# Performance work log

Measured on AMD Instinct MI355X. Metric: run time of the kernel, lower is better.

## Reference

```python
import jax, jax.numpy as jnp
import numpy as np

B, N, D = 1, 65536, 1024
H = 512
R = 16  # num_regions
C = 2   # num_classes

def _gelu(x):
    return jax.nn.gelu(x, approximate=False)  # torch nn.GELU default is exact erf

def setup_inputs() -> dict:
    key = jax.random.key(0)
    ks = jax.random.split(key, 16)
    s = 0.02
    return {
        "embeddings": jax.random.normal(ks[0], (B, N, D), dtype=jnp.float32),
        # region_encoder: Linear(D,H) + GELU (dropout=0 in eval)
        "W1": jax.random.normal(ks[1], (D, H), dtype=jnp.float32) * s,
        "b1": jnp.zeros((H,), dtype=jnp.float32),
        # region_attention: Linear(H,H//2) -> tanh -> Linear(H//2,1)
        "Wa1": jax.random.normal(ks[2], (H, H // 2), dtype=jnp.float32) * s,
        "ba1": jnp.zeros((H // 2,), dtype=jnp.float32),
        "Wa2": jax.random.normal(ks[3], (H // 2, 1), dtype=jnp.float32) * s,
        "ba2": jnp.zeros((1,), dtype=jnp.float32),
        # slide_encoder: Linear(H,H) + GELU
        "Ws": jax.random.normal(ks[4], (H, H), dtype=jnp.float32) * s,
        "bs": jnp.zeros((H,), dtype=jnp.float32),
        # slide_attention
        "Wsa1": jax.random.normal(ks[5], (H, H // 2), dtype=jnp.float32) * s,
        "bsa1": jnp.zeros((H // 2,), dtype=jnp.float32),
        "Wsa2": jax.random.normal(ks[6], (H // 2, 1), dtype=jnp.float32) * s,
        "bsa2": jnp.zeros((1,), dtype=jnp.float32),
        # classifier: Linear(H,H//2) -> GELU -> Linear(H//2,C)
        "Wc1": jax.random.normal(ks[7], (H, H // 2), dtype=jnp.float32) * s,
        "bc1": jnp.zeros((H // 2,), dtype=jnp.float32),
        "Wc2": jax.random.normal(ks[8], (H // 2, C), dtype=jnp.float32) * s,
        "bc2": jnp.zeros((C,), dtype=jnp.float32),
    }

def reference(embeddings, W1, b1, Wa1, ba1, Wa2, ba2, Ws, bs, Wsa1, bsa1, Wsa2, bsa2, Wc1, bc1, Wc2, bc2):
    b, n, d = embeddings.shape
    m = n // R  # patches per region
    # coords=None path: region_ids[i] = i % R, so region r holds indices r, r+R, ...
    # Equivalent regrouping via reshape+transpose: (B, M, R, D) -> (B, R, M, D)
    x = embeddings.reshape(b, m, R, d).transpose(0, 2, 1, 3)
    # region encoder
    region_emb = _gelu(jnp.einsum('brmd,dh->brmh', x, W1) + b1)  # (B,R,M,H)
    # region attention pooling
    scores = jnp.einsum('brmk,ko->brmo', jnp.tanh(jnp.einsum('brmh,hk->brmk', region_emb, Wa1) + ba1), Wa2) + ba2  # (B,R,M,1)
    attn = jax.nn.softmax(scores, axis=2)
    region_features = jnp.sum(region_emb * attn, axis=2)  # (B,R,H)
    # slide encoder + attention pooling over regions
    slide_emb = _gelu(jnp.einsum('brh,hg->brg', region_features, Ws) + bs)  # (B,R,H)
    sattn = jnp.einsum('brk,ko->bro', jnp.tanh(jnp.einsum('brh,hk->brk', slide_emb, Wsa1) + bsa1), Wsa2) + bsa2  # (B,R,1)
    sweights = jax.nn.softmax(sattn, axis=1)
    slide_rep = jnp.sum(slide_emb * sweights, axis=1)  # (B,H)
    # classifier
    logits = _gelu(slide_rep @ Wc1 + bc1) @ Wc2 + bc2  # (B,C)
    return logits
```

## Files before the change

kernel.cpp:

```cpp
#include <hip/hip_runtime.h>

#define NTOK 65536
#define DIN  1024
#define H    512
#define HH   256
#define NREG 16
#define MPR  4096

__device__ __forceinline__ unsigned short f2bf(float f) {
  unsigned u = __float_as_uint(f);
  u += 0x7fffu + ((u >> 16) & 1u);
  return (unsigned short)(u >> 16);
}
__device__ __forceinline__ float bf2f(unsigned short s) {
  return __uint_as_float(((unsigned)s) << 16);
}
__device__ __forceinline__ float gelu_exact(float x) {
  return 0.5f * x * (1.0f + erff(x * 0.70710678118654752440f));
}

typedef __attribute__((ext_vector_type(8))) short shortx8;
typedef __attribute__((ext_vector_type(4))) float floatx4;

__device__ __forceinline__ void gl_lds16(const void* g, void* l) {
  __builtin_amdgcn_global_load_lds(
      (const __attribute__((address_space(1))) void*)g,
      (__attribute__((address_space(3))) void*)l, 16, 0, 0);
}

__global__ __launch_bounds__(256) void k0_prep(const float* __restrict__ W1,
                                               const float* __restrict__ Wa1,
                                               unsigned short* __restrict__ W1t,
                                               unsigned short* __restrict__ Wa1t) {
  int idx = blockIdx.x * 256 + threadIdx.x;
  if (idx < DIN * H) {
    int n = idx >> 10, k = idx & 1023;
    W1t[idx] = f2bf(W1[k * H + n]);
  } else {
    int i2 = idx - DIN * H;
    int n = i2 >> 9, k = i2 & 511;
    Wa1t[i2] = f2bf(Wa1[k * HH + n]);
  }
}

__global__ __launch_bounds__(256) void k1_gemm1(const float* __restrict__ X,
                                                const unsigned short* __restrict__ W1t,
                                                const float* __restrict__ b1,
                                                unsigned short* __restrict__ Eb) {
  __shared__ __align__(16) short lA[128 * 32];
  __shared__ __align__(16) short lB[128 * 32];
  const int tid = threadIdx.x;
  const int colBase = blockIdx.x * 128;
  const int rowBase = blockIdx.y * 128;
  const int lane = tid & 63;
  const int wave = tid >> 6;
  const int wr = wave >> 1, wc = wave & 1;
  const int l15 = lane & 15, quad = lane >> 4;

  floatx4 acc[4][4] = {};

  for (int kb = 0; kb < DIN; kb += 32) {
    __syncthreads();
#pragma unroll
    for (int s = 0; s < 2; s++) {
      int c = tid + s * 256;
      gl_lds16(W1t + (size_t)(colBase + (c >> 2)) * DIN + kb + (c & 3) * 8, &lB[c * 8]);
    }
#pragma unroll
    for (int s = 0; s < 2; s++) {
      int c = tid + s * 256;
      const floatx4* src =
          (const floatx4*)(X + (size_t)(rowBase + (c >> 2)) * DIN + kb + (c & 3) * 8);
      floatx4 f0 = src[0], f1 = src[1];
      shortx8 h;
      h[0] = (short)f2bf(f0[0]); h[1] = (short)f2bf(f0[1]);
      h[2] = (short)f2bf(f0[2]); h[3] = (short)f2bf(f0[3]);
      h[4] = (short)f2bf(f1[0]); h[5] = (short)f2bf(f1[1]);
      h[6] = (short)f2bf(f1[2]); h[7] = (short)f2bf(f1[3]);
      *(shortx8*)(&lA[c * 8]) = h;
    }
    __syncthreads();
    shortx8 aF[4], bF[4];
#pragma unroll
    for (int i = 0; i < 4; i++)
      aF[i] = *(const shortx8*)(&lA[(wr * 64 + i * 16 + l15) * 32 + quad * 8]);
#pragma unroll
    for (int j = 0; j < 4; j++)
      bF[j] = *(const shortx8*)(&lB[(wc * 64 + j * 16 + l15) * 32 + quad * 8]);
#pragma unroll
    for (int i = 0; i < 4; i++)
#pragma unroll
      for (int j = 0; j < 4; j++)
        acc[i][j] = __builtin_amdgcn_mfma_f32_16x16x32_bf16(aF[i], bF[j], acc[i][j], 0, 0, 0);
  }

  const int row0 = rowBase + wr * 64;
  const int col0 = colBase + wc * 64;
#pragma unroll
  for (int j = 0; j < 4; j++) {
    int col = col0 + j * 16 + l15;
    float bias = b1[col];
#pragma unroll
    for (int i = 0; i < 4; i++) {
      int rb = row0 + i * 16 + quad * 4;
#pragma unroll
      for (int v = 0; v < 4; v++) {
        float x = acc[i][j][v] + bias;
        Eb[(size_t)(rb + v) * H + col] = f2bf(gelu_exact(x));
      }
    }
  }
}

__global__ __launch_bounds__(256) void k2_gemm2(const unsigned short* __restrict__ Eb,
                                                const unsigned short* __restrict__ Wa1t,
                                                const float* __restrict__ ba1,
                                                const float* __restrict__ Wa2,
                                                float* __restrict__ scores) {
  __shared__ __align__(16) short lA[128 * 32];
  __shared__ __align__(16) short lB[128 * 32];
  const int tid = threadIdx.x;
  const int colBase = blockIdx.x * 128;
  const int rowBase = blockIdx.y * 128;
  const int lane = tid & 63;
  const int wave = tid >> 6;
  const int wr = wave >> 1, wc = wave & 1;
  const int l15 = lane & 15, quad = lane >> 4;

  floatx4 acc[4][4] = {};

  for (int kb = 0; kb < H; kb += 32) {
    __syncthreads();
#pragma unroll
    for (int s = 0; s < 2; s++) {
      int c = tid + s * 256;
      gl_lds16(Eb + (size_t)(rowBase + (c >> 2)) * H + kb + (c & 3) * 8, &lA[c * 8]);
      gl_lds16(Wa1t + (size_t)(colBase + (c >> 2)) * H + kb + (c & 3) * 8, &lB[c * 8]);
    }
    __syncthreads();
    shortx8 aF[4], bF[4];
#pragma unroll
    for (int i = 0; i < 4; i++)
      aF[i] = *(const shortx8*)(&lA[(wr * 64 + i * 16 + l15) * 32 + quad * 8]);
#pragma unroll
    for (int j = 0; j < 4; j++)
      bF[j] = *(const shortx8*)(&lB[(wc * 64 + j * 16 + l15) * 32 + quad * 8]);
#pragma unroll
    for (int i = 0; i < 4; i++)
#pragma unroll
      for (int j = 0; j < 4; j++)
        acc[i][j] = __builtin_amdgcn_mfma_f32_16x16x32_bf16(aF[i], bF[j], acc[i][j], 0, 0, 0);
  }

  float p[4][4];
#pragma unroll
  for (int i = 0; i < 4; i++)
#pragma unroll
    for (int v = 0; v < 4; v++) p[i][v] = 0.0f;
#pragma unroll
  for (int j = 0; j < 4; j++) {
    int col = colBase + wc * 64 + j * 16 + l15;
    float bias = ba1[col];
    float wa2 = Wa2[col];
#pragma unroll
    for (int i = 0; i < 4; i++)
#pragma unroll
      for (int v = 0; v < 4; v++)
        p[i][v] += tanhf(acc[i][j][v] + bias) * wa2;
  }
#pragma unroll
  for (int i = 0; i < 4; i++)
#pragma unroll
    for (int v = 0; v < 4; v++) {
      float t = p[i][v];
      t += __shfl_xor(t, 1, 16);
      t += __shfl_xor(t, 2, 16);
      t += __shfl_xor(t, 4, 16);
      t += __shfl_xor(t, 8, 16);
      p[i][v] = t;
    }
  if (l15 == 0) {
    int row0 = rowBase + wr * 64 + quad * 4;
#pragma unroll
    for (int i = 0; i < 4; i++)
#pragma unroll
      for (int v = 0; v < 4; v++)
        atomicAdd(&scores[row0 + i * 16 + v], p[i][v]);
  }
}

__global__ __launch_bounds__(256) void k3a_softmax(const float* __restrict__ scores,
                                                   float* __restrict__ wts) {
  const int r = blockIdx.x, tid = threadIdx.x;
  __shared__ float red[256];
  float m = -1e30f;
  for (int j = tid; j < MPR; j += 256) m = fmaxf(m, scores[r + NREG * j]);
  red[tid] = m;
  __syncthreads();
  for (int s = 128; s > 0; s >>= 1) {
    if (tid < s) red[tid] = fmaxf(red[tid], red[tid + s]);
    __syncthreads();
  }
  float mx = red[0];
  __syncthreads();
  float sum = 0.0f;
  for (int j = tid; j < MPR; j += 256) sum += expf(scores[r + NREG * j] - mx);
  red[tid] = sum;
  __syncthreads();
  for (int s = 128; s > 0; s >>= 1) {
    if (tid < s) red[tid] += red[tid + s];
    __syncthreads();
  }
  float inv = 1.0f / red[0];
  for (int j = tid; j < MPR; j += 256)
    wts[r + NREG * j] = expf(scores[r + NREG * j] - mx) * inv;
}

__global__ __launch_bounds__(256) void k3b_wsum(const unsigned short* __restrict__ Eb,
                                                const float* __restrict__ wts,
                                                float* __restrict__ rf) {
  const int r = blockIdx.y;
  const int mc = blockIdx.x;
  const int tid = threadIdx.x;
  float a0 = 0.0f, a1 = 0.0f;
  for (int j = mc * 128; j < mc * 128 + 128; j++) {
    int n = r + NREG * j;
    float w = wts[n];
    unsigned v = *(const unsigned*)(Eb + (size_t)n * H + tid * 2);
    a0 += w * bf2f((unsigned short)(v & 0xffffu));
    a1 += w * bf2f((unsigned short)(v >> 16));
  }
  atomicAdd(&rf[r * H + tid * 2], a0);
  atomicAdd(&rf[r * H + tid * 2 + 1], a1);
}

__global__ __launch_bounds__(256) void k4a_slide(const float* __restrict__ rf,
                                                 const float* __restrict__ Ws,
                                                 const float* __restrict__ bs,
                                                 float* __restrict__ se) {
  const int r = blockIdx.x, tid = threadIdx.x;
  __shared__ float lrf[H];
  lrf[tid] = rf[r * H + tid];
  lrf[tid + 256] = rf[r * H + tid + 256];
  __syncthreads();
  float a0 = 0.0f, a1 = 0.0f;
  for (int k = 0; k < H; k++) {
    float x = lrf[k];
    a0 += x * Ws[k * H + tid];
    a1 += x * Ws[k * H + tid + 256];
  }
  se[r * H + tid] = gelu_exact(a0 + bs[tid]);
  se[r * H + tid + 256] = gelu_exact(a1 + bs[tid + 256]);
}

__global__ __launch_bounds__(256) void k4b_sscore(const float* __restrict__ se,
                                                  const float* __restrict__ Wsa1,
                                                  const float* __restrict__ bsa1,
                                                  const float* __restrict__ Wsa2,
                                                  const float* __restrict__ bsa2,
                                                  float* __restrict__ ss) {
  const int r = blockIdx.x, tid = threadIdx.x;
  __shared__ float lse[H];
  __shared__ float red[256];
  lse[tid] = se[r * H + tid];
  lse[tid + 256] = se[r * H + tid + 256];
  __syncthreads();
  float a = 0.0f;
  for (int k = 0; k < H; k++) a += lse[k] * Wsa1[k * HH + tid];
  red[tid] = tanhf(a + bsa1[tid]) * Wsa2[tid];
  __syncthreads();
  for (int s = 128; s > 0; s >>= 1) {
    if (tid < s) red[tid] += red[tid + s];
    __syncthreads();
  }
  if (tid == 0) ss[r] = red[0] + bsa2[0];
}

__global__ __launch_bounds__(256) void k4c_final(const float* __restrict__ se,
                                                 const float* __restrict__ ss,
                                                 const float* __restrict__ Wc1,
                                                 const float* __restrict__ bc1,
                                                 const float* __restrict__ Wc2,
                                                 const float* __restrict__ bc2,
                                                 float* __restrict__ out) {
  const int tid = threadIdx.x;
  __shared__ float srep[H];
  __shared__ float r0[256], r1[256];
  float mx = -1e30f;
  for (int i = 0; i < NREG; i++) mx = fmaxf(mx, ss[i]);
  float wv[NREG];
  float den = 0.0f;
  for (int i = 0; i < NREG; i++) { wv[i] = expf(ss[i] - mx); den += wv[i]; }
  float inv = 1.0f / den;
  float s0 = 0.0f, s1 = 0.0f;
  for (int i = 0; i < NREG; i++) {
    float w = wv[i] * inv;
    s0 += w * se[i * H + tid];
    s1 += w * se[i * H + tid + 256];
  }
  srep[tid] = s0;
  srep[tid + 256] = s1;
  __syncthreads();
  float a = 0.0f;
  for (int k = 0; k < H; k++) a += srep[k] * Wc1[k * HH + tid];
  float g = gelu_exact(a + bc1[tid]);
  r0[tid] = g * Wc2[tid * 2];
  r1[tid] = g * Wc2[tid * 2 + 1];
  __syncthreads();
  for (int s = 128; s > 0; s >>= 1) {
    if (tid < s) { r0[tid] += r0[tid + s]; r1[tid] += r1[tid + s]; }
    __syncthreads();
  }
  if (tid == 0) {
    out[0] = r0[0] + bc2[0];
    out[1] = r1[0] + bc2[1];
  }
}

extern "C" void kernel_launch(void* const* d_in, const int* in_sizes, int n_in,
                              void* d_out, int out_size, void* d_ws, size_t ws_size,
                              hipStream_t stream) {
  const float* X    = (const float*)d_in[0];
  const float* W1   = (const float*)d_in[1];
  const float* b1   = (const float*)d_in[2];
  const float* Wa1  = (const float*)d_in[3];
  const float* ba1  = (const float*)d_in[4];
  const float* Wa2  = (const float*)d_in[5];
  const float* Ws   = (const float*)d_in[7];
  const float* bs   = (const float*)d_in[8];
  const float* Wsa1 = (const float*)d_in[9];
  const float* bsa1 = (const float*)d_in[10];
  const float* Wsa2 = (const float*)d_in[11];
  const float* bsa2 = (const float*)d_in[12];
  const float* Wc1  = (const float*)d_in[13];
  const float* bc1  = (const float*)d_in[14];
  const float* Wc2  = (const float*)d_in[15];
  const float* bc2  = (const float*)d_in[16];
  float* out = (float*)d_out;

  char* ws = (char*)d_ws;
  constexpr size_t OFF_W1T  = 0;
  constexpr size_t OFF_WA1T = OFF_W1T + (size_t)H * DIN * 2;
  constexpr size_t OFF_EB   = OFF_WA1T + (size_t)HH * H * 2;
  constexpr size_t OFF_SC   = OFF_EB + (size_t)NTOK * H * 2;
  constexpr size_t OFF_RF   = OFF_SC + (size_t)NTOK * 4;
  constexpr size_t OFF_WT   = OFF_RF + (size_t)NREG * H * 4;
  constexpr size_t OFF_SE   = OFF_WT + (size_t)NTOK * 4;
  constexpr size_t OFF_SS   = OFF_SE + (size_t)NREG * H * 4;

  unsigned short* W1t  = (unsigned short*)(ws + OFF_W1T);
  unsigned short* Wa1t = (unsigned short*)(ws + OFF_WA1T);
  unsigned short* Eb   = (unsigned short*)(ws + OFF_EB);
  float* scores = (float*)(ws + OFF_SC);
  float* rf     = (float*)(ws + OFF_RF);
  float* wts    = (float*)(ws + OFF_WT);
  float* se     = (float*)(ws + OFF_SE);
  float* ssb    = (float*)(ws + OFF_SS);

  hipMemsetAsync(scores, 0, (size_t)NTOK * 4 + (size_t)NREG * H * 4, stream);

  k0_prep<<<(DIN * H + HH * H) / 256, 256, 0, stream>>>(W1, Wa1, W1t, Wa1t);
  k1_gemm1<<<dim3(4, 512), 256, 0, stream>>>(X, W1t, b1, Eb);
  k2_gemm2<<<dim3(2, 512), 256, 0, stream>>>(Eb, Wa1t, ba1, Wa2, scores);
  k3a_softmax<<<NREG, 256, 0, stream>>>(scores, wts);
  k3b_wsum<<<dim3(32, NREG), 256, 0, stream>>>(Eb, wts, rf);
  k4a_slide<<<NREG, 256, 0, stream>>>(rf, Ws, bs, se);
  k4b_sscore<<<NREG, 256, 0, stream>>>(se, Wsa1, bsa1, Wsa2, bsa2, ssb);
  k4c_final<<<1, 256, 0, stream>>>(se, ssb, Wc1, bc1, Wc2, bc2, out);
}
```

Before: 652.6 us.

## Widen GEMM1 tile to full H, swizzle LDS, use hardware bf16 convert and fast tanh

GEMM1 now uses 512-thread blocks that each compute a 128x512 output tile, so every block covers all of H. Each fp32 X row is then read and converted once instead of four times. LDS layouts in both GEMMs get an XOR swizzle to reduce bank conflicts on fragment reads. Hardware v_cvt_pk_bf16_f32 replaces the software rounding, and an exp/rcp tanh replaces tanhf in the score epilogue. The costs are much higher register pressure from 32 accumulators per wave, a larger LDS footprint, and a slightly less accurate tanh.

```diff
diff --git a/kernel.cpp b/kernel.cpp
--- a/kernel.cpp
+++ b/kernel.cpp
@@ -18,14 +18,33 @@
 __device__ __forceinline__ float gelu_exact(float x) {
   return 0.5f * x * (1.0f + erff(x * 0.70710678118654752440f));
 }
+__device__ __forceinline__ unsigned cvt_pk_bf16(float lo, float hi) {
+  unsigned r;
+  asm("v_cvt_pk_bf16_f32 %0, %1, %2" : "=v"(r) : "v"(lo), "v"(hi));
+  return r;
+}
+__device__ __forceinline__ unsigned short f2bf_hw(float f) {
+  unsigned r;
+  asm("v_cvt_pk_bf16_f32 %0, %1, %2" : "=v"(r) : "v"(f), "v"(f));
+  return (unsigned short)r;
+}
+__device__ __forceinline__ float fast_tanh(float x) {
+  float e = __expf(2.0f * x);
+  return 1.0f - 2.0f * __builtin_amdgcn_rcpf(e + 1.0f);
+}
 
 typedef __attribute__((ext_vector_type(8))) short shortx8;
 typedef __attribute__((ext_vector_type(4))) float floatx4;
+typedef __attribute__((ext_vector_type(4))) unsigned int uintx4;
 
 __device__ __forceinline__ void gl_lds16(const void* g, void* l) {
   __builtin_amdgcn_global_load_lds(
       (const __attribute__((address_space(1))) void*)g,
       (__attribute__((address_space(3))) void*)l, 16, 0, 0);
+}
+
+__device__ __forceinline__ int swz8(int row, int seg) {
+  return (row * 4 + (seg ^ ((row >> 1) & 3))) * 8;
 }
 
 __global__ __launch_bounds__(256) void k0_prep(const float* __restrict__ W1,
@@ -43,62 +62,67 @@
   }
 }
 
-__global__ __launch_bounds__(256) void k1_gemm1(const float* __restrict__ X,
+__global__ __launch_bounds__(512) void k1_gemm1(const float* __restrict__ X,
                                                 const unsigned short* __restrict__ W1t,
                                                 const float* __restrict__ b1,
                                                 unsigned short* __restrict__ Eb) {
   __shared__ __align__(16) short lA[128 * 32];
-  __shared__ __align__(16) short lB[128 * 32];
+  __shared__ __align__(16) short lB[512 * 32];
   const int tid = threadIdx.x;
-  const int colBase = blockIdx.x * 128;
-  const int rowBase = blockIdx.y * 128;
+  const int rowBase = blockIdx.x * 128;
   const int lane = tid & 63;
   const int wave = tid >> 6;
-  const int wr = wave >> 1, wc = wave & 1;
+  const int wr = wave >> 2, wc = wave & 3;
   const int l15 = lane & 15, quad = lane >> 4;
 
-  floatx4 acc[4][4] = {};
+  floatx4 acc[4][8] = {};
+
+  const int arow = tid >> 2, aseg = tid & 3;
+  const float* aSrc = X + (size_t)(rowBase + arow) * DIN + aseg * 8;
+  short* aDst = &lA[swz8(arow, aseg)];
 
   for (int kb = 0; kb < DIN; kb += 32) {
     __syncthreads();
 #pragma unroll
-    for (int s = 0; s < 2; s++) {
-      int c = tid + s * 256;
-      gl_lds16(W1t + (size_t)(colBase + (c >> 2)) * DIN + kb + (c & 3) * 8, &lB[c * 8]);
-    }
-#pragma unroll
-    for (int s = 0; s < 2; s++) {
-      int c = tid + s * 256;
-      const floatx4* src =
-          (const floatx4*)(X + (size_t)(rowBase + (c >> 2)) * DIN + kb + (c & 3) * 8);
+    for (int s = 0; s < 4; s++) {
+      int c = tid + s * 512;
+      int n = c >> 2, slot = c & 3;
+      int seg = slot ^ ((n >> 1) & 3);
+      gl_lds16(W1t + (size_t)n * DIN + kb + seg * 8, &lB[c * 8]);
+    }
+    {
+      const floatx4* src = (const floatx4*)(aSrc + kb);
       floatx4 f0 = src[0], f1 = src[1];
-      shortx8 h;
-      h[0] = (short)f2bf(f0[0]); h[1] = (short)f2bf(f0[1]);
-      h[2] = (short)f2bf(f0[2]); h[3] = (short)f2bf(f0[3]);
-      h[4] = (short)f2bf(f1[0]); h[5] = (short)f2bf(f1[1]);
-      h[6] = (short)f2bf(f1[2]); h[7] = (short)f2bf(f1[3]);
-      *(shortx8*)(&lA[c * 8]) = h;
-    }
-    __syncthreads();
-    shortx8 aF[4], bF[4];
+      uintx4 u;
+      u[0] = cvt_pk_bf16(f0[0], f0[1]);
+      u[1] = cvt_pk_bf16(f0[2], f0[3]);
+      u[2] = cvt_pk_bf16(f1[0], f1[1]);
+      u[3] = cvt_pk_bf16(f1[2], f1[3]);
+      *(uintx4*)aDst = u;
+    }
+    __syncthreads();
+    shortx8 aF[4], bF[8];
+#pragma unroll
+    for (int i = 0; i < 4; i++) {
+      int r = wr * 64 + i * 16 + l15;
+      aF[i] = *(const shortx8*)(&lA[swz8(r, quad)]);
+    }
+#pragma unroll
+    for (int j = 0; j < 8; j++) {
+      int r = wc * 128 + j * 16 + l15;
+      bF[j] = *(const shortx8*)(&lB[swz8(r, quad)]);
+    }
 #pragma unroll
     for (int i = 0; i < 4; i++)
-      aF[i] = *(const shortx8*)(&lA[(wr * 64 + i * 16 + l15) * 32 + quad * 8]);
-#pragma unroll
-    for (int j = 0; j < 4; j++)
-      bF[j] = *(const shortx8*)(&lB[(wc * 64 + j * 16 + l15) * 32 + quad * 8]);
-#pragma unroll
-    for (int i = 0; i < 4; i++)
-#pragma unroll
-      for (int j = 0; j < 4; j++)
+#pragma unroll
+      for (int j = 0; j < 8; j++)
         acc[i][j] = __builtin_amdgcn_mfma_f32_16x16x32_bf16(aF[i], bF[j], acc[i][j], 0, 0, 0);
   }
 
   const int row0 = rowBase + wr * 64;
-  const int col0 = colBase + wc * 64;
-#pragma unroll
-  for (int j = 0; j < 4; j++) {
-    int col = col0 + j * 16 + l15;
+#pragma unroll
+  for (int j = 0; j < 8; j++) {
+    int col = wc * 128 + j * 16 + l15;
     float bias = b1[col];
 #pragma unroll
     for (int i = 0; i < 4; i++) {
@@ -106,7 +130,7 @@
 #pragma unroll
       for (int v = 0; v < 4; v++) {
         float x = acc[i][j][v] + bias;
-        Eb[(size_t)(rb + v) * H + col] = f2bf(gelu_exact(x));
+        Eb[(size_t)(rb + v) * H + col] = f2bf_hw(gelu_exact(x));
       }
     }
   }
@@ -134,17 +158,23 @@
 #pragma unroll
     for (int s = 0; s < 2; s++) {
       int c = tid + s * 256;
-      gl_lds16(Eb + (size_t)(rowBase + (c >> 2)) * H + kb + (c & 3) * 8, &lA[c * 8]);
-      gl_lds16(Wa1t + (size_t)(colBase + (c >> 2)) * H + kb + (c & 3) * 8, &lB[c * 8]);
+      int n = c >> 2, slot = c & 3;
+      int seg = slot ^ ((n >> 1) & 3);
+      gl_lds16(Eb + (size_t)(rowBase + n) * H + kb + seg * 8, &lA[c * 8]);
+      gl_lds16(Wa1t + (size_t)(colBase + n) * H + kb + seg * 8, &lB[c * 8]);
     }
     __syncthreads();
     shortx8 aF[4], bF[4];
 #pragma unroll
-    for (int i = 0; i < 4; i++)
-      aF[i] = *(const shortx8*)(&lA[(wr * 64 + i * 16 + l15) * 32 + quad * 8]);
-#pragma unroll
-    for (int j = 0; j < 4; j++)
-      bF[j] = *(const shortx8*)(&lB[(wc * 64 + j * 16 + l15) * 32 + quad * 8]);
+    for (int i = 0; i < 4; i++) {
+      int r = wr * 64 + i * 16 + l15;
+      aF[i] = *(const shortx8*)(&lA[swz8(r, quad)]);
+    }
+#pragma unroll
+    for (int j = 0; j < 4; j++) {
+      int r = wc * 64 + j * 16 + l15;
+      bF[j] = *(const shortx8*)(&lB[swz8(r, quad)]);
+    }
 #pragma unroll
     for (int i = 0; i < 4; i++)
 #pragma unroll
@@ -166,7 +196,7 @@
     for (int i = 0; i < 4; i++)
 #pragma unroll
       for (int v = 0; v < 4; v++)
-        p[i][v] += tanhf(acc[i][j][v] + bias) * wa2;
+        p[i][v] += fast_tanh(acc[i][j][v] + bias) * wa2;
   }
 #pragma unroll
   for (int i = 0; i < 4; i++)
@@ -360,7 +390,7 @@
   hipMemsetAsync(scores, 0, (size_t)NTOK * 4 + (size_t)NREG * H * 4, stream);
 
   k0_prep<<<(DIN * H + HH * H) / 256, 256, 0, stream>>>(W1, Wa1, W1t, Wa1t);
-  k1_gemm1<<<dim3(4, 512), 256, 0, stream>>>(X, W1t, b1, Eb);
+  k1_gemm1<<<512, 512, 0, stream>>>(X, W1t, b1, Eb);
   k2_gemm2<<<dim3(2, 512), 256, 0, stream>>>(Eb, Wa1t, ba1, Wa2, scores);
   k3a_softmax<<<NREG, 256, 0, stream>>>(scores, wts);
   k3b_wsum<<<dim3(32, NREG), 256, 0, stream>>>(Eb, wts, rf);
```

Result: faster. 619.1 us (-5.1%).
